# Performance work log

Hardware: AMD Instinct MI355X
Metric: run time of the kernel (lower is better)

The kernel has to match this reference:

```python
import jax, jax.numpy as jnp
import numpy as np

N_QUBITS = 10
Q_DEPTH = 6


def _apply_1q(state, gate, wire):
    """Apply a 2x2 gate (or batched [B,2,2] gates) to `wire` of state [B,2,...,2]."""
    s = jnp.moveaxis(state, wire + 1, -1)
    if gate.ndim == 2:
        s = s @ gate.T  # new_j = sum_i G[j,i] * old_i
    else:
        s = jnp.einsum('b...i,bji->b...j', s, gate)
    return jnp.moveaxis(s, -1, wire + 1)


def _apply_cnot(state, ctrl, tgt):
    s = jnp.moveaxis(state, (ctrl + 1, tgt + 1), (-2, -1))
    s = jnp.stack([s[..., 0, :], s[..., 1, ::-1]], axis=-2)  # flip target where ctrl=1
    return jnp.moveaxis(s, (-2, -1), (ctrl + 1, tgt + 1))


def _ry(theta):
    """RY(theta) = [[cos(t/2), -sin(t/2)], [sin(t/2), cos(t/2)]]; theta scalar or [B]."""
    c, s = jnp.cos(theta / 2.0), jnp.sin(theta / 2.0)
    return jnp.stack([jnp.stack([c, -s], -1), jnp.stack([s, c], -1)], -2)


def _vqc(angles, q_weights):
    """angles: [B, n_qubits] per-sample RY angles; q_weights: [q_depth, n_qubits].
    Returns <PauliZ_w> for every wire: [B, n_qubits]. All gates are real -> float32 state."""
    B, n = angles.shape
    q_depth = q_weights.shape[0]
    # H-layer on |0...0> gives the uniform superposition: all amplitudes 2^{-n/2}
    state = jnp.full((B,) + (2,) * n, 2.0 ** (-n / 2.0), dtype=angles.dtype)
    # RY layer with per-sample input angles
    for w in range(n):
        state = _apply_1q(state, _ry(angles[:, w]), w)
    # q_depth x (brick-wall CNOT entangler + trainable RY layer)
    for k in range(q_depth):
        for i in range(0, n - 1, 2):
            state = _apply_cnot(state, i, i + 1)
        for i in range(1, n - 1, 2):
            state = _apply_cnot(state, i, i + 1)
        for w in range(n):
            state = _apply_1q(state, _ry(q_weights[k, w]), w)
    # expval(PauliZ(w)) = P(wire w = 0) - P(wire w = 1)
    probs = state * state  # real statevector
    exps = []
    for w in range(n):
        p = jnp.moveaxis(probs, w + 1, 1).reshape(B, 2, -1).sum(-1)
        exps.append(p[:, 0] - p[:, 1])
    return jnp.stack(exps, -1)


def setup_inputs() -> dict:
    key = jax.random.key(0)
    ks = jax.random.split(key, 6)
    B, D_IN, OUT = 8192, 512, 64
    x = jax.random.normal(ks[0], (B, D_IN), dtype=jnp.float32)
    W1 = jax.random.normal(ks[1], (D_IN, N_QUBITS), dtype=jnp.float32) * (1.0 / np.sqrt(D_IN))
    b1 = jnp.zeros((N_QUBITS,), dtype=jnp.float32)
    # keras 'uniform' initializer: U(-0.05, 0.05)
    q_weights = jax.random.uniform(ks[2], (Q_DEPTH, N_QUBITS), dtype=jnp.float32,
                                   minval=-0.05, maxval=0.05)
    W2 = jax.random.normal(ks[3], (N_QUBITS, OUT), dtype=jnp.float32) * (1.0 / np.sqrt(N_QUBITS))
    b2 = jnp.zeros((OUT,), dtype=jnp.float32)
    return {"x": x, "W1": W1, "b1": b1, "q_weights": q_weights, "W2": W2, "b2": b2}


def reference(x, W1, b1, q_weights, W2, b2):
    # Dense(n_qubits, tanh) then scale to angles in (-pi/2, pi/2)
    angles = jnp.tanh(x @ W1 + b1) * (jnp.pi / 2.0)  # [B, n_qubits]
    q_out = _vqc(angles, q_weights)                   # [B, n_qubits]
    return q_out @ W2 + b2                            # [B, output_dim]
```

## Files before the change

### kernel.cpp

```cpp
#include <hip/hip_runtime.h>

#define NQ 10
#define QD 6
#define DIN 512
#define DOUT 64

template <int CTRL>
__device__ __forceinline__ float dppf(float v) {
    return __int_as_float(__builtin_amdgcn_mov_dpp(__float_as_int(v), CTRL, 0xF, 0xF, true));
}
template <int M>
__device__ __forceinline__ float sx(float v) {
    if constexpr (M == 1)       return dppf<0xB1>(v);
    else if constexpr (M == 2)  return dppf<0x4E>(v);
    else if constexpr (M == 4)  return dppf<0x1B>(dppf<0x141>(v));
    else                        return dppf<0x128>(v);
}

#if __has_builtin(__builtin_amdgcn_permlane32_swap)
__device__ __forceinline__ void pl32(float& a, float& b) {
    auto r = __builtin_amdgcn_permlane32_swap(__float_as_int(a), __float_as_int(b), false, false);
    a = __int_as_float(r[0]); b = __int_as_float(r[1]);
}
#else
__device__ __forceinline__ void pl32(float& a, float& b) {
    const int lane = threadIdx.x & 63;
    const int xaddr = ((threadIdx.x ^ 32) & 63) << 2;
    const float pa = __int_as_float(__builtin_amdgcn_ds_bpermute(xaddr, __float_as_int(a)));
    const float pb = __int_as_float(__builtin_amdgcn_ds_bpermute(xaddr, __float_as_int(b)));
    const bool hi = (lane & 32) != 0;
    const float na = hi ? pb : a;
    const float nb = hi ? b  : pa;
    a = na; b = nb;
}
#endif
#if __has_builtin(__builtin_amdgcn_permlane16_swap)
__device__ __forceinline__ void pl16(float& a, float& b) {
    auto r = __builtin_amdgcn_permlane16_swap(__float_as_int(a), __float_as_int(b), false, false);
    a = __int_as_float(r[0]); b = __int_as_float(r[1]);
}
#else
__device__ __forceinline__ void pl16(float& a, float& b) {
    const int lane = threadIdx.x & 63;
    const float pa = __int_as_float(__builtin_amdgcn_ds_swizzle(__float_as_int(a), 0x401F));
    const float pb = __int_as_float(__builtin_amdgcn_ds_swizzle(__float_as_int(b), 0x401F));
    const bool odd = (lane & 16) != 0;
    const float na = odd ? pb : a;
    const float nb = odd ? b  : pa;
    a = na; b = nb;
}
#endif

__device__ __forceinline__ void gate_pl32(float& u, float& v, float T) {
    pl32(u, v);
    float n0 = fmaf(-T, v, u);
    float n1 = fmaf( T, u, v);
    pl32(n0, n1);
    u = n0; v = n1;
}
__device__ __forceinline__ void gate_pl16(float& u, float& v, float T, bool cswap) {
    pl16(u, v);
    const float q0 = fmaf(-T, v, u);
    const float q1 = fmaf( T, u, v);
    float n0 = cswap ? q1 : q0;
    float n1 = cswap ? q0 : q1;
    pl16(n0, n1);
    u = n0; v = n1;
}

__device__ __forceinline__ float rowred(float v) {
    v += dppf<0x128>(v); v += dppf<0x124>(v);
    v += dppf<0x122>(v); v += dppf<0x121>(v);
    return v;
}
__device__ __forceinline__ void fin4(float& a, float& b, float& c, float& d) {
    pl16(a, b); float z0 = a + b;
    pl16(c, d); float z1 = c + d;
    pl32(z0, z1); float t = z0 + z1;
    float u = t; pl32(t, u);
    b = t; pl16(t, b); a = t;
    d = u; pl16(u, d); c = u;
}
__device__ __forceinline__ void fin2(float& a, float& b) {
    pl16(a, b); float z = a + b;
    float z2 = z; pl32(z, z2); float t = z + z2;
    b = t; pl16(t, b); a = t;
}

__device__ __forceinline__ float tanh_fast(float x) {
    const float e = __expf(2.0f * x);
    return 1.0f - __fdividef(2.0f, e + 1.0f);
}

__global__ __launch_bounds__(256) void dqc_main(
    const float* __restrict__ x,
    const float* __restrict__ W1,
    const float* __restrict__ b1,
    const float* __restrict__ qw,
    const float* __restrict__ W2,
    const float* __restrict__ b2,
    float* __restrict__ out,
    const int B)
{
    __shared__ __align__(16) float csl[QD * 24];
    __shared__ __align__(16) float tsl[QD * 8];

    const int tid = threadIdx.x;
    if (tid < QD * NQ) {
        const int layer = tid / NQ, wire = tid - layer * NQ;
        const float h = qw[tid] * 0.5f;
        const float s = __sinf(h), c = __cosf(h);
        const int pos = layer * 24 + (wire & 1) * 12 + (wire >> 1) * 2;
        csl[pos] = c; csl[pos + 1] = s;
        int slot = -1;
        if (wire == 0) slot = 0; else if (wire == 7) slot = 1;
        else if (wire == 8) slot = 2; else if (wire == 9) slot = 3;
        else if (wire == 1) slot = 4; else if (wire == 3) slot = 5;
        else if (wire == 5) slot = 6;
        if (slot >= 0) tsl[layer * 8 + slot] = __fdividef(s, c);
    }

    const int lane = tid & 63;
    const int b = blockIdx.x * 4 + (tid >> 6);
    const int bb = (b < B) ? b : (B - 1);

    float xr[8];
    {
        const float4* xp = (const float4*)(x + (size_t)bb * DIN + lane * 8);
        const float4 v0 = xp[0], v1 = xp[1];
        xr[0]=v0.x; xr[1]=v0.y; xr[2]=v0.z; xr[3]=v0.w;
        xr[4]=v1.x; xr[5]=v1.y; xr[6]=v1.z; xr[7]=v1.w;
    }
    float dot[NQ];
    #pragma unroll
    for (int w = 0; w < NQ; ++w) dot[w] = 0.f;
    {
        const float4* wp = (const float4*)(W1 + (size_t)lane * 8 * NQ);
        #pragma unroll
        for (int j = 0; j < 4; ++j) {
            const float4 f0 = wp[5*j], f1 = wp[5*j+1], f2 = wp[5*j+2],
                         f3 = wp[5*j+3], f4 = wp[5*j+4];
            const float xa = xr[2*j], xb = xr[2*j+1];
            dot[0]=fmaf(xa,f0.x,dot[0]); dot[1]=fmaf(xa,f0.y,dot[1]);
            dot[2]=fmaf(xa,f0.z,dot[2]); dot[3]=fmaf(xa,f0.w,dot[3]);
            dot[4]=fmaf(xa,f1.x,dot[4]); dot[5]=fmaf(xa,f1.y,dot[5]);
            dot[6]=fmaf(xa,f1.z,dot[6]); dot[7]=fmaf(xa,f1.w,dot[7]);
            dot[8]=fmaf(xa,f2.x,dot[8]); dot[9]=fmaf(xa,f2.y,dot[9]);
            dot[0]=fmaf(xb,f2.z,dot[0]); dot[1]=fmaf(xb,f2.w,dot[1]);
            dot[2]=fmaf(xb,f3.x,dot[2]); dot[3]=fmaf(xb,f3.y,dot[3]);
            dot[4]=fmaf(xb,f3.z,dot[4]); dot[5]=fmaf(xb,f3.w,dot[5]);
            dot[6]=fmaf(xb,f4.x,dot[6]); dot[7]=fmaf(xb,f4.y,dot[7]);
            dot[8]=fmaf(xb,f4.z,dot[8]); dot[9]=fmaf(xb,f4.w,dot[9]);
        }
    }
    #pragma unroll
    for (int w = 0; w < NQ; ++w) dot[w] = rowred(dot[w]);
    fin4(dot[0], dot[1], dot[2], dot[3]);
    fin4(dot[4], dot[5], dot[6], dot[7]);
    fin2(dot[8], dot[9]);

    float u0[NQ], u1[NQ];
    #pragma unroll
    for (int w = 0; w < NQ; ++w) {
        const float phi = fmaf(tanh_fast(dot[w] + b1[w]),
                               0.78539816339744830962f, 0.78539816339744830962f);
        u0[w] = __cosf(phi);
        u1[w] = __sinf(phi);
    }

    __syncthreads();

    float F = 1.f;
    #pragma unroll
    for (int k = 0; k < QD; ++k) {
        const float* ce = csl + k * 24;
        F *= ce[0] * ce[18];
        F *= ce[8] * ce[20];
        F *= ce[12];
    }
    {   const float* c5 = csl + 5 * 24;
        F *= c5[14] * c5[16];
    }

    float A[16];
    {
        float lf = ((lane & 32) ? u1[0] : u0[0]);
        lf *= ((((lane >> 4) ^ (lane >> 5)) & 1) ? u1[1] : u0[1]);
        lf *= ((lane & 8) ? u1[2] : u0[2]);
        lf *= ((((lane >> 2) ^ (lane >> 3)) & 1) ? u1[3] : u0[3]);
        lf *= ((lane & 2) ? u1[4] : u0[4]);
        lf *= (((lane ^ (lane >> 1)) & 1) ? u1[5] : u0[5]);
        lf *= F;
        float d1[2] = { lf * u0[6], lf * u1[6] };
        float d2[4], d3[8];
        #pragma unroll
        for (int i = 0; i < 4; ++i) {
            const int r3 = i >> 1, r2 = i & 1;
            d2[i] = d1[r3] * (((r2 ^ r3) & 1) ? u1[7] : u0[7]);
        }
        #pragma unroll
        for (int i = 0; i < 8; ++i)
            d3[i] = d2[i >> 1] * ((i & 1) ? u1[8] : u0[8]);
        #pragma unroll
        for (int i = 0; i < 8; ++i) {
            const int r1 = i & 1;
            A[2*i]   = d3[i] * (r1 ? u1[9] : u0[9]);
            A[2*i+1] = d3[i] * (r1 ? u0[9] : u1[9]);
        }
    }

    #pragma unroll 1
    for (int k = 0; k < QD; ++k) {
        const float* ce = csl + k * 24;
        const float4 ea = *(const float4*)(ce);
        const float4 eb = *(const float4*)(ce + 4);
        const float4 tv = *(const float4*)(tsl + k * 8);
        const float4 tw = *(const float4*)(tsl + k * 8 + 4);
        const float C2=ea.z,S2=ea.w, C4=eb.x,S4=eb.y, C6=eb.z,S6=eb.w;
        const float T0=tv.x, T7=tv.y, T8=tv.z, T9=tv.w;
        const float T1=tw.x;

        {
            #pragma unroll
            for (int i = 0; i < 8; ++i)
                gate_pl32(A[2*i], A[2*i+1], T0);
        }
        {
            const float g = (lane & 8) ? S2 : -S2;
            const bool cb = (lane & 16) != 0;
            const float al = cb ? g : C2, be = cb ? C2 : g;
            #pragma unroll
            for (int r = 0; r < 16; ++r) A[r] = fmaf(al, A[r], be * sx<8>(A[r]));
        }
        {
            const float g = (lane & 2) ? S4 : -S4;
            const bool cb = (lane & 4) != 0;
            const float al = cb ? g : C4, be = cb ? C4 : g;
            #pragma unroll
            for (int r = 0; r < 16; ++r) A[r] = fmaf(al, A[r], be * sx<2>(A[r]));
        }
        {
            const bool cb = (lane & 1) != 0;
            const float a_lo = cb ? -S6 : C6, b_lo = cb ? C6 : -S6;
            const float a_hi = cb ?  S6 : C6, b_hi = cb ? C6 :  S6;
            #pragma unroll
            for (int r = 0; r < 8; ++r) {
                const float lo = A[r], hi = A[r + 8];
                A[r]     = fmaf(a_lo, lo, b_lo * hi);
                A[r + 8] = fmaf(a_hi, hi, b_hi * lo);
            }
        }
        {
            #pragma unroll
            for (int r = 0; r < 16; ++r) {
                if (r & 2) continue;
                const float lo = A[r], hi = A[r + 2];
                if (r & 4) {
                    A[r]     = fmaf(-T8, lo, hi);
                    A[r + 2] = fmaf( T8, hi, lo);
                } else {
                    A[r]     = fmaf(-T8, hi, lo);
                    A[r + 2] = fmaf( T8, lo, hi);
                }
            }
        }

        if (k != QD - 1) {
            const float4 oa = *(const float4*)(ce + 12);
            const float2 ob = *(const float2*)(ce + 16);
            const float C3=oa.z,S3=oa.w, C5=ob.x,S5=ob.y;

            {
                const bool cb = (lane & 32) != 0;
                #pragma unroll
                for (int i = 0; i < 8; ++i)
                    gate_pl16(A[2*i], A[2*i+1], T1, cb);
            }
            {
                const float g = (lane & 4) ? S3 : -S3;
                const bool cb = (lane & 8) != 0;
                const float al = cb ? -g : C3, be = cb ? C3 : g;
                #pragma unroll
                for (int r = 0; r < 16; ++r) A[r] = fmaf(al, A[r], be * sx<4>(A[r]));
            }
            {
                const float g = (lane & 1) ? S5 : -S5;
                const bool cb = (lane & 2) != 0;
                const float al = cb ? -g : C5, be = cb ? C5 : g;
                #pragma unroll
                for (int r = 0; r < 16; ++r) A[r] = fmaf(al, A[r], be * sx<1>(A[r]));
            }
            {
                #pragma unroll
                for (int r = 0; r < 16; ++r) {
                    if (r & 4) continue;
                    const float lo = A[r], hi = A[r + 4];
                    if (r & 8) {
                        A[r]     = fmaf( T7, lo, hi);
                        A[r + 4] = fmaf(-T7, hi, lo);
                    } else {
                        A[r]     = fmaf(-T7, hi, lo);
                        A[r + 4] = fmaf( T7, lo, hi);
                    }
                }
            }
            {
                #pragma unroll
                for (int r = 0; r < 16; r += 2) {
                    const float xv = A[r], yv = A[r + 1];
                    if (r & 2) {
                        A[r]     = fmaf( T9, xv, yv);
                        A[r + 1] = fmaf(-T9, yv, xv);
                    } else {
                        A[r]     = fmaf(-T9, yv, xv);
                        A[r + 1] = fmaf( T9, xv, yv);
                    }
                }
            }
        } else {
            const float T3 = tw.y, T5 = tw.z;

            {
                #pragma unroll
                for (int i = 0; i < 8; ++i)
                    gate_pl16(A[2*i], A[2*i+1], T1, false);
            }
            {
                const float t3 = (lane & 4) ? T3 : -T3;
                #pragma unroll
                for (int r = 0; r < 16; ++r) A[r] = fmaf(t3, sx<4>(A[r]), A[r]);
            }
            {
                const float t5 = (lane & 1) ? T5 : -T5;
                #pragma unroll
                for (int r = 0; r < 16; ++r) A[r] = fmaf(t5, sx<1>(A[r]), A[r]);
            }
            {
                #pragma unroll
                for (int r = 0; r < 16; ++r) {
                    if (r & 4) continue;
                    const float lo = A[r], hi = A[r + 4];
                    A[r]     = fmaf(-T7, hi, lo);
                    A[r + 4] = fmaf( T7, lo, hi);
                }
            }
            {
                #pragma unroll
                for (int r = 0; r < 16; r += 2) {
                    const float xv = A[r], yv = A[r + 1];
                    A[r]     = fmaf(-T9, yv, xv);
                    A[r + 1] = fmaf( T9, xv, yv);
                }
            }
        }
    }

    float tot = 0.f, q6 = 0.f, q7 = 0.f, q8 = 0.f, q9 = 0.f;
    #pragma unroll
    for (int r = 0; r < 16; ++r) {
        const float P = A[r] * A[r];
        tot += P;
        if (r & 8) q6 += P;
        if (r & 4) q7 += P;
        if (r & 2) q8 += P;
        if (r & 1) q9 += P;
    }
    float e[NQ];
    e[0] = (lane & 32) ? -tot : tot;
    e[1] = (lane & 16) ? -tot : tot;
    e[2] = (lane & 8)  ? -tot : tot;
    e[3] = (lane & 4)  ? -tot : tot;
    e[4] = (lane & 2)  ? -tot : tot;
    e[5] = (lane & 1)  ? -tot : tot;
    e[6] = fmaf(-2.f, q6, tot);
    e[7] = fmaf(-2.f, q7, tot);
    e[8] = fmaf(-2.f, q8, tot);
    e[9] = fmaf(-2.f, q9, tot);
    #pragma unroll
    for (int w = 0; w < NQ; ++w) e[w] = rowred(e[w]);
    fin4(e[0], e[1], e[2], e[3]);
    fin4(e[4], e[5], e[6], e[7]);
    fin2(e[8], e[9]);

    if (b < B) {
        float o = b2[lane];
        #pragma unroll
        for (int w = 0; w < NQ; ++w) o = fmaf(e[w], W2[w * DOUT + lane], o);
        out[(size_t)b * DOUT + lane] = o;
    }
}

extern "C" void kernel_launch(void* const* d_in, const int* in_sizes, int n_in,
                              void* d_out, int out_size, void* d_ws, size_t ws_size,
                              hipStream_t stream) {
    const float* x  = (const float*)d_in[0];
    const float* W1 = (const float*)d_in[1];
    const float* b1 = (const float*)d_in[2];
    const float* qw = (const float*)d_in[3];
    const float* W2 = (const float*)d_in[4];
    const float* b2 = (const float*)d_in[5];
    float* out = (float*)d_out;

    const int B = in_sizes[0] / DIN;
    const int blocks = (B + 3) / 4;
    dqc_main<<<blocks, 256, 0, stream>>>(x, W1, b1, qw, W2, b2, out, B);
}
```

Before: 106.3 us.

## Replace DPP and permlane-swap gate exchanges with ds_swizzle and ds_bpermute lane shuffles

Switches the cross-lane exchanges in the statevector gate loop from DPP moves and paired permlane16/32 swaps to LDS-crossbar ds_swizzle (xor masks) and ds_bpermute. The wire-0 and wire-1 gates now use a single lane exchange with a sign-folded FMA instead of swap, compute, swap back. Wire 1 also drops the factored tangent form in the intermediate layers, taking the cos factor out of F and using full cos/sin coefficients. This cuts the number of shuffle instructions, but ds_swizzle and ds_bpermute go through the LDS path and have higher latency than DPP, so throughput may suffer.

```diff
diff --git a/kernel.cpp b/kernel.cpp
--- a/kernel.cpp
+++ b/kernel.cpp
@@ -9,12 +9,12 @@
 __device__ __forceinline__ float dppf(float v) {
     return __int_as_float(__builtin_amdgcn_mov_dpp(__float_as_int(v), CTRL, 0xF, 0xF, true));
 }
-template <int M>
-__device__ __forceinline__ float sx(float v) {
-    if constexpr (M == 1)       return dppf<0xB1>(v);
-    else if constexpr (M == 2)  return dppf<0x4E>(v);
-    else if constexpr (M == 4)  return dppf<0x1B>(dppf<0x141>(v));
-    else                        return dppf<0x128>(v);
+template <int MASK>
+__device__ __forceinline__ float swz(float v) {
+    return __int_as_float(__builtin_amdgcn_ds_swizzle(__float_as_int(v), MASK));
+}
+__device__ __forceinline__ float bperm(float v, int xaddr) {
+    return __int_as_float(__builtin_amdgcn_ds_bpermute(xaddr, __float_as_int(v)));
 }
 
 #if __has_builtin(__builtin_amdgcn_permlane32_swap)
@@ -26,8 +26,8 @@
 __device__ __forceinline__ void pl32(float& a, float& b) {
     const int lane = threadIdx.x & 63;
     const int xaddr = ((threadIdx.x ^ 32) & 63) << 2;
-    const float pa = __int_as_float(__builtin_amdgcn_ds_bpermute(xaddr, __float_as_int(a)));
-    const float pb = __int_as_float(__builtin_amdgcn_ds_bpermute(xaddr, __float_as_int(b)));
+    const float pa = bperm(a, xaddr);
+    const float pb = bperm(b, xaddr);
     const bool hi = (lane & 32) != 0;
     const float na = hi ? pb : a;
     const float nb = hi ? b  : pa;
@@ -42,31 +42,14 @@
 #else
 __device__ __forceinline__ void pl16(float& a, float& b) {
     const int lane = threadIdx.x & 63;
-    const float pa = __int_as_float(__builtin_amdgcn_ds_swizzle(__float_as_int(a), 0x401F));
-    const float pb = __int_as_float(__builtin_amdgcn_ds_swizzle(__float_as_int(b), 0x401F));
+    const float pa = swz<0x401F>(a);
+    const float pb = swz<0x401F>(b);
     const bool odd = (lane & 16) != 0;
     const float na = odd ? pb : a;
     const float nb = odd ? b  : pa;
     a = na; b = nb;
 }
 #endif
-
-__device__ __forceinline__ void gate_pl32(float& u, float& v, float T) {
-    pl32(u, v);
-    float n0 = fmaf(-T, v, u);
-    float n1 = fmaf( T, u, v);
-    pl32(n0, n1);
-    u = n0; v = n1;
-}
-__device__ __forceinline__ void gate_pl16(float& u, float& v, float T, bool cswap) {
-    pl16(u, v);
-    const float q0 = fmaf(-T, v, u);
-    const float q1 = fmaf( T, u, v);
-    float n0 = cswap ? q1 : q0;
-    float n1 = cswap ? q0 : q1;
-    pl16(n0, n1);
-    u = n0; v = n1;
-}
 
 __device__ __forceinline__ float rowred(float v) {
     v += dppf<0x128>(v); v += dppf<0x124>(v);
@@ -123,6 +106,7 @@
     const int lane = tid & 63;
     const int b = blockIdx.x * 4 + (tid >> 6);
     const int bb = (b < B) ? b : (B - 1);
+    const int xaddr = ((tid ^ 32) & 63) << 2;
 
     float xr[8];
     {
@@ -176,10 +160,10 @@
         const float* ce = csl + k * 24;
         F *= ce[0] * ce[18];
         F *= ce[8] * ce[20];
-        F *= ce[12];
     }
     {   const float* c5 = csl + 5 * 24;
-        F *= c5[14] * c5[16];
+        F *= c5[12] * c5[14];
+        F *= c5[16];
     }
 
     float A[16];
@@ -215,29 +199,30 @@
         const float4 ea = *(const float4*)(ce);
         const float4 eb = *(const float4*)(ce + 4);
         const float4 tv = *(const float4*)(tsl + k * 8);
-        const float4 tw = *(const float4*)(tsl + k * 8 + 4);
         const float C2=ea.z,S2=ea.w, C4=eb.x,S4=eb.y, C6=eb.z,S6=eb.w;
         const float T0=tv.x, T7=tv.y, T8=tv.z, T9=tv.w;
-        const float T1=tw.x;
 
         {
-            #pragma unroll
-            for (int i = 0; i < 8; ++i)
-                gate_pl32(A[2*i], A[2*i+1], T0);
+            const float t0 = (lane & 32) ? T0 : -T0;
+            float p[16];
+            #pragma unroll
+            for (int r = 0; r < 16; ++r) p[r] = bperm(A[r], xaddr);
+            #pragma unroll
+            for (int r = 0; r < 16; ++r) A[r] = fmaf(t0, p[r], A[r]);
         }
         {
             const float g = (lane & 8) ? S2 : -S2;
             const bool cb = (lane & 16) != 0;
             const float al = cb ? g : C2, be = cb ? C2 : g;
             #pragma unroll
-            for (int r = 0; r < 16; ++r) A[r] = fmaf(al, A[r], be * sx<8>(A[r]));
+            for (int r = 0; r < 16; ++r) A[r] = fmaf(al, A[r], be * swz<0x201F>(A[r]));
         }
         {
             const float g = (lane & 2) ? S4 : -S4;
             const bool cb = (lane & 4) != 0;
             const float al = cb ? g : C4, be = cb ? C4 : g;
             #pragma unroll
-            for (int r = 0; r < 16; ++r) A[r] = fmaf(al, A[r], be * sx<2>(A[r]));
+            for (int r = 0; r < 16; ++r) A[r] = fmaf(al, A[r], be * swz<0x081F>(A[r]));
         }
         {
             const bool cb = (lane & 1) != 0;
@@ -268,27 +253,31 @@
         if (k != QD - 1) {
             const float4 oa = *(const float4*)(ce + 12);
             const float2 ob = *(const float2*)(ce + 16);
-            const float C3=oa.z,S3=oa.w, C5=ob.x,S5=ob.y;
-
-            {
+            const float C1=oa.x,S1=oa.y, C3=oa.z,S3=oa.w, C5=ob.x,S5=ob.y;
+
+            {
+                const float g = (lane & 16) ? S1 : -S1;
                 const bool cb = (lane & 32) != 0;
-                #pragma unroll
-                for (int i = 0; i < 8; ++i)
-                    gate_pl16(A[2*i], A[2*i+1], T1, cb);
+                const float al = cb ? -g : C1, be = cb ? C1 : g;
+                float p[16];
+                #pragma unroll
+                for (int r = 0; r < 16; ++r) p[r] = swz<0x401F>(A[r]);
+                #pragma unroll
+                for (int r = 0; r < 16; ++r) A[r] = fmaf(al, A[r], be * p[r]);
             }
             {
                 const float g = (lane & 4) ? S3 : -S3;
                 const bool cb = (lane & 8) != 0;
                 const float al = cb ? -g : C3, be = cb ? C3 : g;
                 #pragma unroll
-                for (int r = 0; r < 16; ++r) A[r] = fmaf(al, A[r], be * sx<4>(A[r]));
+                for (int r = 0; r < 16; ++r) A[r] = fmaf(al, A[r], be * swz<0x101F>(A[r]));
             }
             {
                 const float g = (lane & 1) ? S5 : -S5;
                 const bool cb = (lane & 2) != 0;
                 const float al = cb ? -g : C5, be = cb ? C5 : g;
                 #pragma unroll
-                for (int r = 0; r < 16; ++r) A[r] = fmaf(al, A[r], be * sx<1>(A[r]));
+                for (int r = 0; r < 16; ++r) A[r] = fmaf(al, A[r], be * swz<0x041F>(A[r]));
             }
             {
                 #pragma unroll
@@ -318,22 +307,26 @@
                 }
             }
         } else {
-            const float T3 = tw.y, T5 = tw.z;
-
-            {
-                #pragma unroll
-                for (int i = 0; i < 8; ++i)
-                    gate_pl16(A[2*i], A[2*i+1], T1, false);
+            const float4 tv2 = *(const float4*)(tsl + k * 8 + 4);
+            const float T1 = tv2.x, T3 = tv2.y, T5 = tv2.z;
+
+            {
+                const float t1 = (lane & 16) ? T1 : -T1;
+                float p[16];
+                #pragma unroll
+                for (int r = 0; r < 16; ++r) p[r] = swz<0x401F>(A[r]);
+                #pragma unroll
+                for (int r = 0; r < 16; ++r) A[r] = fmaf(t1, p[r], A[r]);
             }
             {
                 const float t3 = (lane & 4) ? T3 : -T3;
                 #pragma unroll
-                for (int r = 0; r < 16; ++r) A[r] = fmaf(t3, sx<4>(A[r]), A[r]);
+                for (int r = 0; r < 16; ++r) A[r] = fmaf(t3, swz<0x101F>(A[r]), A[r]);
             }
             {
                 const float t5 = (lane & 1) ? T5 : -T5;
                 #pragma unroll
-                for (int r = 0; r < 16; ++r) A[r] = fmaf(t5, sx<1>(A[r]), A[r]);
+                for (int r = 0; r < 16; ++r) A[r] = fmaf(t5, swz<0x041F>(A[r]), A[r]);
             }
             {
                 #pragma unroll
```

Result: faster. 100.7 us (-5.3%).
